# Performance work log

Hardware: AMD Instinct MI355X
Metric: run time of the kernel (lower is better)

The kernel has to match this reference:

```python
import jax, jax.numpy as jnp
import numpy as np
from jax import lax

K_NN = 16      # neighbors used by compute_knn_distance
ANCHOR_K = 64  # config['anchor_k']


def _knn_dist_vec(pts):
    """compute_knn_distance for one object: mean offset vector to K_NN nearest neighbors.
    pts: (N, 3) -> (N, 3)"""
    sq = jnp.sum(pts * pts, axis=-1)                      # (N,)
    d2 = sq[:, None] + sq[None, :] - 2.0 * (pts @ pts.T)  # (N, N) squared dists
    n = pts.shape[0]
    d2 = d2 + jnp.eye(n, dtype=pts.dtype) * 1e10          # exclude self
    _, idx = lax.top_k(-d2, K_NN)                          # (N, K_NN) nearest indices
    neigh = pts[idx]                                       # (N, K_NN, 3)
    return jnp.mean(neigh - pts[:, None, :], axis=1)       # (N, 3)


def _fps(pts, k):
    """Farthest point sampling for one object. pts: (N, 3) -> (k,) int32 indices."""
    d0 = jnp.sum((pts - pts[0]) ** 2, axis=-1)             # dist to seed point 0

    def step(min_d, _):
        idx = jnp.argmax(min_d)
        d = jnp.sum((pts - pts[idx]) ** 2, axis=-1)
        return jnp.minimum(min_d, d), idx

    _, idxs = lax.scan(step, d0, None, length=k - 1)
    return jnp.concatenate([jnp.zeros((1,), dtype=idxs.dtype), idxs])


def setup_inputs() -> dict:
    key = jax.random.key(0)
    k1, k2, k3, k4 = jax.random.split(key, 4)
    B, N_obj, N_v = 4, 8, 2048
    positions = jax.random.normal(k1, (B, N_obj, N_v, 3), dtype=jnp.float32)
    velocities = jax.random.normal(k2, (B, N_obj, N_v, 3), dtype=jnp.float32)
    physics_params = jax.random.uniform(k3, (B, N_obj, 3), dtype=jnp.float32)
    # reference pose at t=0: nearby but distinct so rel_pos is nontrivial
    ref_positions = positions + 0.05 * jax.random.normal(k4, (B, N_obj, N_v, 3), dtype=jnp.float32)
    return {"positions": positions, "velocities": velocities,
            "physics_params": physics_params, "ref_positions": ref_positions}


def reference(positions, velocities, physics_params, ref_positions):
    B, N_obj, N_v, _ = positions.shape
    flat = positions.reshape(B * N_obj, N_v, 3)

    # pairwise KNN distance feature per point
    dist_vec = jax.vmap(_knn_dist_vec)(flat).reshape(B, N_obj, N_v, 3)

    # iterative FPS anchor sampling (vectorized over all B*N_obj objects)
    anchors = jax.vmap(lambda p: _fps(p, ANCHOR_K))(flat).reshape(B, N_obj, ANCHOR_K)

    rel_pos = positions - ref_positions

    # multi-field gather at anchor indices (torch.gather on dim=2)
    gather = lambda f: jnp.take_along_axis(f, anchors[..., None], axis=2)
    anchor_dist = gather(dist_vec)       # (B, N_obj, K, 3)
    anchor_vel = gather(velocities)      # (B, N_obj, K, 3)
    anchor_rel = gather(rel_pos)         # (B, N_obj, K, 3)

    phys = jnp.broadcast_to(physics_params[:, :, None, :], (B, N_obj, ANCHOR_K, 3))
    query = jnp.concatenate([anchor_dist, anchor_vel, anchor_rel, phys], axis=-1)  # (B, N_obj, K, 12)
    return query
```

## Files before the change

### kernel.cpp

```cpp
#include <hip/hip_runtime.h>
#include <stdint.h>

#define NPTS 2048
#define KNN  16
#define AK   64
#define TPB  256
#define FPT  (NPTS / TPB)
#define KPL  (NPTS / 64)

typedef unsigned long long u64;
typedef unsigned int u32;
#define UMAX 0xFFFFFFFFFFFFFFFFull

__device__ __forceinline__ float sq3(float x, float y, float z) {
    return __fadd_rn(__fadd_rn(__fmul_rn(x, x), __fmul_rn(y, y)), __fmul_rn(z, z));
}

template <int CTRL>
__device__ __forceinline__ u64 dpp64(u64 k) {
    const int lo = __builtin_amdgcn_update_dpp((int)(u32)k, (int)(u32)k,
                                               CTRL, 0xF, 0xF, false);
    const int hi = __builtin_amdgcn_update_dpp((int)(u32)(k >> 32),
                                               (int)(u32)(k >> 32),
                                               CTRL, 0xF, 0xF, false);
    return ((u64)(u32)hi << 32) | (u32)lo;
}

__device__ __forceinline__ u64 wave_max64(u64 k) {
    u64 o;
    o = dpp64<0xB1>(k);  if (o > k) k = o;
    o = dpp64<0x4E>(k);  if (o > k) k = o;
    o = dpp64<0x141>(k); if (o > k) k = o;
    o = dpp64<0x140>(k); if (o > k) k = o;
    o = (u64)__shfl_xor((long long)k, 16, 64); if (o > k) k = o;
    o = (u64)__shfl_xor((long long)k, 32, 64); if (o > k) k = o;
    return k;
}

__device__ __forceinline__ u64 wave_min64(u64 k) {
    u64 o;
    o = dpp64<0xB1>(k);  if (o < k) k = o;
    o = dpp64<0x4E>(k);  if (o < k) k = o;
    o = dpp64<0x141>(k); if (o < k) k = o;
    o = dpp64<0x140>(k); if (o < k) k = o;
    o = (u64)__shfl_xor((long long)k, 16, 64); if (o < k) k = o;
    o = (u64)__shfl_xor((long long)k, 32, 64); if (o < k) k = o;
    return k;
}

__global__ __launch_bounds__(TPB) void fps_kernel(const float* __restrict__ pos,
                                                  int* __restrict__ anchors) {
    const int obj = blockIdx.x;
    const int t = threadIdx.x;
    const int wid = t >> 6, lane = t & 63;

    __shared__ float sX[NPTS], sY[NPTS], sZ[NPTS];
    __shared__ u64 skey[8];
    __shared__ float4 scrd[8];

    const float* pts = pos + (size_t)obj * NPTS * 3;
    #pragma unroll
    for (int i = 0; i < FPT; i++) {
        const int j = t + i * TPB;
        sX[j] = pts[j * 3 + 0];
        sY[j] = pts[j * 3 + 1];
        sZ[j] = pts[j * 3 + 2];
    }
    __syncthreads();

    float px[FPT], py[FPT], pz[FPT], mind[FPT];
    u64 key;
    {
        const float ax0 = sX[0], ay0 = sY[0], az0 = sZ[0];
        float bv = -1.0f; u32 bj = 0;
        #pragma unroll
        for (int i = 0; i < FPT; i++) {
            const int j = t + i * TPB;
            px[i] = sX[j]; py[i] = sY[j]; pz[i] = sZ[j];
            const float d2 = sq3(__fsub_rn(px[i], ax0), __fsub_rn(py[i], ay0),
                                 __fsub_rn(pz[i], az0));
            mind[i] = d2;
            if (d2 > bv) { bv = d2; bj = (u32)j; }
        }
        key = ((u64)__float_as_uint(bv) << 32) | (u32)(~bj);
    }
    if (t == 0) anchors[obj * AK + 0] = 0;

    for (int s = 1; s < AK; s++) {
        const u64 wk = wave_max64(key);
        const int side = (s & 1) * 4;
        if (lane == 0) {
            const int widx = (int)(~(u32)wk);
            skey[side + wid] = wk;
            scrd[side + wid] = make_float4(sX[widx], sY[widx], sZ[widx], 0.f);
        }
        __syncthreads();
        u64 ka = skey[side + 0];
        float4 ca = scrd[side + 0];
        { const u64 k1 = skey[side + 1]; const float4 q = scrd[side + 1];
          if (k1 > ka) { ka = k1; ca = q; } }
        { const u64 k2 = skey[side + 2]; const float4 q = scrd[side + 2];
          if (k2 > ka) { ka = k2; ca = q; } }
        { const u64 k3 = skey[side + 3]; const float4 q = scrd[side + 3];
          if (k3 > ka) { ka = k3; ca = q; } }
        if (t == 0) anchors[obj * AK + s] = (int)(~(u32)ka);
        if (s == AK - 1) break;

        float bv = -1.0f; u32 bj = 0;
        #pragma unroll
        for (int i = 0; i < FPT; i++) {
            const float d2 = sq3(__fsub_rn(px[i], ca.x), __fsub_rn(py[i], ca.y),
                                 __fsub_rn(pz[i], ca.z));
            const float nm = fminf(mind[i], d2);
            mind[i] = nm;
            if (nm > bv) { bv = nm; bj = (u32)(t + i * TPB); }
        }
        key = ((u64)__float_as_uint(bv) << 32) | (u32)(~bj);
    }
}

__global__ __launch_bounds__(TPB) void knn_gather_kernel(
    const float* __restrict__ pos, const float* __restrict__ vel,
    const float* __restrict__ phys, const float* __restrict__ refp,
    const int* __restrict__ anchors, float* __restrict__ out) {
    const int t = threadIdx.x;
    const int wid = t >> 6, lane = t & 63;
    const int g = blockIdx.x * 4 + wid;
    const int obj = g >> 6;

    __shared__ float sX[NPTS], sY[NPTS], sZ[NPTS];
    const float* pts = pos + (size_t)obj * NPTS * 3;
    #pragma unroll
    for (int i = 0; i < FPT; i++) {
        const int j = t + i * TPB;
        sX[j] = pts[j * 3 + 0];
        sY[j] = pts[j * 3 + 1];
        sZ[j] = pts[j * 3 + 2];
    }
    const int a = anchors[g];
    __syncthreads();

    const float ax = sX[a], ay = sY[a], az = sZ[a];
    const float sqa = sq3(ax, ay, az);

    u64 k[KPL];
    #pragma unroll
    for (int i = 0; i < KPL; i++) {
        const int j = lane + i * 64;
        const float x = sX[j], y = sY[j], z = sZ[j];
        const float sqj = sq3(x, y, z);
        const float dot = __fadd_rn(
            __fadd_rn(__fmul_rn(ax, x), __fmul_rn(ay, y)), __fmul_rn(az, z));
        const float d2 = __fsub_rn(__fadd_rn(sqa, sqj), __fmul_rn(2.0f, dot));
        u32 bb = __float_as_uint(d2);
        bb ^= (bb & 0x80000000u) ? 0xFFFFFFFFu : 0x80000000u;
        k[i] = (j == a) ? UMAX : (((u64)bb << 32) | (u32)j);
    }

    u64 c0 = UMAX, c1 = UMAX, c2 = UMAX, c3 = UMAX;
    #pragma unroll
    for (int i = 0; i < KPL; i++) c0 = (k[i] < c0) ? k[i] : c0;
    #pragma unroll
    for (int i = 0; i < KPL; i++) {
        const u64 v = (k[i] > c0) ? k[i] : UMAX; c1 = (v < c1) ? v : c1;
    }
    #pragma unroll
    for (int i = 0; i < KPL; i++) {
        const u64 v = (k[i] > c1) ? k[i] : UMAX; c2 = (v < c2) ? v : c2;
    }
    #pragma unroll
    for (int i = 0; i < KPL; i++) {
        const u64 v = (k[i] > c2) ? k[i] : UMAX; c3 = (v < c3) ? v : c3;
    }

    float accx = 0.f, accy = 0.f, accz = 0.f;
    u64 thr = 0;
    for (int r = 0; r < KNN; r++) {
        if (c0 == UMAX) {
            #pragma unroll
            for (int i = 0; i < KPL; i++) {
                const u64 v = (k[i] > thr) ? k[i] : UMAX; c0 = (v < c0) ? v : c0;
            }
            #pragma unroll
            for (int i = 0; i < KPL; i++) {
                const u64 v = (k[i] > c0) ? k[i] : UMAX; c1 = (v < c1) ? v : c1;
            }
            #pragma unroll
            for (int i = 0; i < KPL; i++) {
                const u64 v = (k[i] > c1) ? k[i] : UMAX; c2 = (v < c2) ? v : c2;
            }
            #pragma unroll
            for (int i = 0; i < KPL; i++) {
                const u64 v = (k[i] > c2) ? k[i] : UMAX; c3 = (v < c3) ? v : c3;
            }
        }
        const u64 w = wave_min64(c0);
        const int winj = (int)(u32)w;
        const float wx = sX[winj], wy = sY[winj], wz = sZ[winj];
        accx = __fadd_rn(accx, __fsub_rn(wx, ax));
        accy = __fadd_rn(accy, __fsub_rn(wy, ay));
        accz = __fadd_rn(accz, __fsub_rn(wz, az));
        if (c0 == w) {
            thr = c0; c0 = c1; c1 = c2; c2 = c3; c3 = UMAX;
        }
    }

    if (lane == 0) {
        float* o = out + (size_t)g * 12;
        o[0] = __fmul_rn(accx, 0.0625f);
        o[1] = __fmul_rn(accy, 0.0625f);
        o[2] = __fmul_rn(accz, 0.0625f);
        const size_t base = (size_t)obj * NPTS * 3 + (size_t)a * 3;
        o[3] = vel[base + 0];
        o[4] = vel[base + 1];
        o[5] = vel[base + 2];
        o[6] = __fsub_rn(pos[base + 0], refp[base + 0]);
        o[7] = __fsub_rn(pos[base + 1], refp[base + 1]);
        o[8] = __fsub_rn(pos[base + 2], refp[base + 2]);
        const float* ph = phys + (size_t)obj * 3;
        o[9]  = ph[0];
        o[10] = ph[1];
        o[11] = ph[2];
    }
}

extern "C" void kernel_launch(void* const* d_in, const int* in_sizes, int n_in,
                              void* d_out, int out_size, void* d_ws, size_t ws_size,
                              hipStream_t stream) {
    const float* pos  = (const float*)d_in[0];
    const float* vel  = (const float*)d_in[1];
    const float* phys = (const float*)d_in[2];
    const float* refp = (const float*)d_in[3];
    float* out = (float*)d_out;

    const int n_obj = in_sizes[2] / 3;
    int* anchors = (int*)d_ws;

    fps_kernel<<<n_obj, TPB, 0, stream>>>(pos, anchors);
    knn_gather_kernel<<<n_obj * AK / 4, TPB, 0, stream>>>(pos, vel, phys, refp,
                                                          anchors, out);
}
```

Measured before the change: 109.6 us.

## Carry winner coordinates through DPP reductions, pack float2 math, shrink KNN candidate cache

The FPS kernel no longer stages points in shared memory. It loads each thread's points straight into registers as float2 pairs and carries the winning point's coordinates through the wave max reduction, so the per-step shared-memory coordinate lookup goes away. Wave reductions now use DPP row_bcast with readlane instead of shfl_xor. The KNN kernel computes distances with packed float2 math and keeps two cached candidates per lane instead of four, which cuts the initial selection passes but may trigger more rescans.

```diff
diff --git a/kernel.cpp b/kernel.cpp
--- a/kernel.cpp
+++ b/kernel.cpp
@@ -5,59 +5,157 @@
 #define KNN  16
 #define AK   64
 #define TPB  256
-#define FPT  (NPTS / TPB)
-#define KPL  (NPTS / 64)
+#define FPT  8
+#define FPP  4
+#define KPL  32
+#define KPP  16
 
 typedef unsigned long long u64;
 typedef unsigned int u32;
+typedef __attribute__((ext_vector_type(2))) float v2f;
 #define UMAX 0xFFFFFFFFFFFFFFFFull
 
 __device__ __forceinline__ float sq3(float x, float y, float z) {
     return __fadd_rn(__fadd_rn(__fmul_rn(x, x), __fmul_rn(y, y)), __fmul_rn(z, z));
 }
 
-template <int CTRL>
-__device__ __forceinline__ u64 dpp64(u64 k) {
-    const int lo = __builtin_amdgcn_update_dpp((int)(u32)k, (int)(u32)k,
-                                               CTRL, 0xF, 0xF, false);
-    const int hi = __builtin_amdgcn_update_dpp((int)(u32)(k >> 32),
-                                               (int)(u32)(k >> 32),
-                                               CTRL, 0xF, 0xF, false);
-    return ((u64)(u32)hi << 32) | (u32)lo;
-}
-
-__device__ __forceinline__ u64 wave_max64(u64 k) {
-    u64 o;
-    o = dpp64<0xB1>(k);  if (o > k) k = o;
-    o = dpp64<0x4E>(k);  if (o > k) k = o;
-    o = dpp64<0x141>(k); if (o > k) k = o;
-    o = dpp64<0x140>(k); if (o > k) k = o;
-    o = (u64)__shfl_xor((long long)k, 16, 64); if (o > k) k = o;
-    o = (u64)__shfl_xor((long long)k, 32, 64); if (o > k) k = o;
-    return k;
+template <int CTRL, int RMASK>
+__device__ __forceinline__ u32 dpp32(u32 v) {
+    return (u32)__builtin_amdgcn_update_dpp((int)v, (int)v, CTRL, RMASK, 0xF, false);
+}
+
+template <int CTRL, int RMASK>
+__device__ __forceinline__ void maxstep(u32& lo, u32& hi,
+                                        float& x, float& y, float& z) {
+    const u32 olo = dpp32<CTRL, RMASK>(lo);
+    const u32 ohi = dpp32<CTRL, RMASK>(hi);
+    const u32 ox = dpp32<CTRL, RMASK>(__float_as_uint(x));
+    const u32 oy = dpp32<CTRL, RMASK>(__float_as_uint(y));
+    const u32 oz = dpp32<CTRL, RMASK>(__float_as_uint(z));
+    const u64 a = ((u64)hi << 32) | lo;
+    const u64 b = ((u64)ohi << 32) | olo;
+    if (b > a) {
+        lo = olo; hi = ohi;
+        x = __uint_as_float(ox); y = __uint_as_float(oy); z = __uint_as_float(oz);
+    }
+}
+
+template <int CTRL, int RMASK>
+__device__ __forceinline__ u64 minstep(u64 k) {
+    const u32 olo = dpp32<CTRL, RMASK>((u32)k);
+    const u32 ohi = dpp32<CTRL, RMASK>((u32)(k >> 32));
+    const u64 o = ((u64)ohi << 32) | olo;
+    return (o < k) ? o : k;
 }
 
 __device__ __forceinline__ u64 wave_min64(u64 k) {
-    u64 o;
-    o = dpp64<0xB1>(k);  if (o < k) k = o;
-    o = dpp64<0x4E>(k);  if (o < k) k = o;
-    o = dpp64<0x141>(k); if (o < k) k = o;
-    o = dpp64<0x140>(k); if (o < k) k = o;
-    o = (u64)__shfl_xor((long long)k, 16, 64); if (o < k) k = o;
-    o = (u64)__shfl_xor((long long)k, 32, 64); if (o < k) k = o;
-    return k;
+    k = minstep<0xB1, 0xF>(k);
+    k = minstep<0x4E, 0xF>(k);
+    k = minstep<0x141, 0xF>(k);
+    k = minstep<0x140, 0xF>(k);
+    k = minstep<0x142, 0xA>(k);
+    k = minstep<0x143, 0xC>(k);
+    const u32 lo = (u32)__builtin_amdgcn_readlane((int)(u32)k, 63);
+    const u32 hi = (u32)__builtin_amdgcn_readlane((int)(u32)(k >> 32), 63);
+    return ((u64)hi << 32) | lo;
 }
 
 __global__ __launch_bounds__(TPB) void fps_kernel(const float* __restrict__ pos,
                                                   int* __restrict__ anchors) {
+#pragma clang fp contract(off)
     const int obj = blockIdx.x;
     const int t = threadIdx.x;
     const int wid = t >> 6, lane = t & 63;
-
-    __shared__ float sX[NPTS], sY[NPTS], sZ[NPTS];
+    const float* pts = pos + (size_t)obj * NPTS * 3;
+
     __shared__ u64 skey[8];
     __shared__ float4 scrd[8];
 
+    v2f px[FPP], py[FPP], pz[FPP], mind[FPP];
+    float bv, bx, by, bz;
+    u32 bj;
+    {
+        const float ax0 = pts[0], ay0 = pts[1], az0 = pts[2];
+        bv = -1.0f; bj = 0; bx = by = bz = 0.0f;
+        #pragma unroll
+        for (int i = 0; i < FPP; i++) {
+            const int jA = t + (2 * i) * TPB;
+            const int jB = t + (2 * i + 1) * TPB;
+            v2f X, Y, Z;
+            X.x = pts[jA * 3 + 0]; Y.x = pts[jA * 3 + 1]; Z.x = pts[jA * 3 + 2];
+            X.y = pts[jB * 3 + 0]; Y.y = pts[jB * 3 + 1]; Z.y = pts[jB * 3 + 2];
+            px[i] = X; py[i] = Y; pz[i] = Z;
+            const v2f dx = X - ax0, dy = Y - ay0, dz = Z - az0;
+            const v2f d2 = dx * dx + dy * dy + dz * dz;
+            mind[i] = d2;
+            if (d2.x > bv) { bv = d2.x; bj = (u32)jA; bx = X.x; by = Y.x; bz = Z.x; }
+            if (d2.y > bv) { bv = d2.y; bj = (u32)jB; bx = X.y; by = Y.y; bz = Z.y; }
+        }
+    }
+    if (t == 0) anchors[obj * AK + 0] = 0;
+
+    for (int s = 1; s < AK; s++) {
+        u32 klo = ~bj, khi = __float_as_uint(bv);
+        float wx = bx, wy = by, wz = bz;
+        maxstep<0xB1, 0xF>(klo, khi, wx, wy, wz);
+        maxstep<0x4E, 0xF>(klo, khi, wx, wy, wz);
+        maxstep<0x141, 0xF>(klo, khi, wx, wy, wz);
+        maxstep<0x140, 0xF>(klo, khi, wx, wy, wz);
+        maxstep<0x142, 0xA>(klo, khi, wx, wy, wz);
+        maxstep<0x143, 0xC>(klo, khi, wx, wy, wz);
+        const u32 wlo = (u32)__builtin_amdgcn_readlane((int)klo, 63);
+        const u32 whi = (u32)__builtin_amdgcn_readlane((int)khi, 63);
+        const u32 ux = (u32)__builtin_amdgcn_readlane((int)__float_as_uint(wx), 63);
+        const u32 uy = (u32)__builtin_amdgcn_readlane((int)__float_as_uint(wy), 63);
+        const u32 uz = (u32)__builtin_amdgcn_readlane((int)__float_as_uint(wz), 63);
+
+        const int side = (s & 1) * 4;
+        if (lane == 0) {
+            skey[side + wid] = ((u64)whi << 32) | wlo;
+            scrd[side + wid] = make_float4(__uint_as_float(ux), __uint_as_float(uy),
+                                           __uint_as_float(uz), 0.0f);
+        }
+        __syncthreads();
+
+        u64 ka = skey[side + 0];
+        float4 ca = scrd[side + 0];
+        { const u64 kb = skey[side + 1]; const float4 cb = scrd[side + 1];
+          if (kb > ka) { ka = kb; ca = cb; } }
+        { const u64 kb = skey[side + 2]; const float4 cb = scrd[side + 2];
+          if (kb > ka) { ka = kb; ca = cb; } }
+        { const u64 kb = skey[side + 3]; const float4 cb = scrd[side + 3];
+          if (kb > ka) { ka = kb; ca = cb; } }
+        if (t == 0) anchors[obj * AK + s] = (int)(~(u32)ka);
+        if (s == AK - 1) break;
+
+        bv = -1.0f; bj = 0;
+        #pragma unroll
+        for (int i = 0; i < FPP; i++) {
+            const v2f dx = px[i] - ca.x, dy = py[i] - ca.y, dz = pz[i] - ca.z;
+            const v2f d2 = dx * dx + dy * dy + dz * dz;
+            v2f nm;
+            nm.x = fminf(mind[i].x, d2.x);
+            nm.y = fminf(mind[i].y, d2.y);
+            mind[i] = nm;
+            if (nm.x > bv) { bv = nm.x; bj = (u32)(t + (2 * i) * TPB);
+                             bx = px[i].x; by = py[i].x; bz = pz[i].x; }
+            if (nm.y > bv) { bv = nm.y; bj = (u32)(t + (2 * i + 1) * TPB);
+                             bx = px[i].y; by = py[i].y; bz = pz[i].y; }
+        }
+    }
+}
+
+__global__ __launch_bounds__(TPB) void knn_gather_kernel(
+    const float* __restrict__ pos, const float* __restrict__ vel,
+    const float* __restrict__ phys, const float* __restrict__ refp,
+    const int* __restrict__ anchors, float* __restrict__ out) {
+#pragma clang fp contract(off)
+    const int t = threadIdx.x;
+    const int wid = t >> 6, lane = t & 63;
+    const int g = blockIdx.x * 4 + wid;
+    const int obj = g >> 6;
+
+    __shared__ float sX[NPTS], sY[NPTS], sZ[NPTS];
     const float* pts = pos + (size_t)obj * NPTS * 3;
     #pragma unroll
     for (int i = 0; i < FPT; i++) {
@@ -66,77 +164,6 @@
         sY[j] = pts[j * 3 + 1];
         sZ[j] = pts[j * 3 + 2];
     }
-    __syncthreads();
-
-    float px[FPT], py[FPT], pz[FPT], mind[FPT];
-    u64 key;
-    {
-        const float ax0 = sX[0], ay0 = sY[0], az0 = sZ[0];
-        float bv = -1.0f; u32 bj = 0;
-        #pragma unroll
-        for (int i = 0; i < FPT; i++) {
-            const int j = t + i * TPB;
-            px[i] = sX[j]; py[i] = sY[j]; pz[i] = sZ[j];
-            const float d2 = sq3(__fsub_rn(px[i], ax0), __fsub_rn(py[i], ay0),
-                                 __fsub_rn(pz[i], az0));
-            mind[i] = d2;
-            if (d2 > bv) { bv = d2; bj = (u32)j; }
-        }
-        key = ((u64)__float_as_uint(bv) << 32) | (u32)(~bj);
-    }
-    if (t == 0) anchors[obj * AK + 0] = 0;
-
-    for (int s = 1; s < AK; s++) {
-        const u64 wk = wave_max64(key);
-        const int side = (s & 1) * 4;
-        if (lane == 0) {
-            const int widx = (int)(~(u32)wk);
-            skey[side + wid] = wk;
-            scrd[side + wid] = make_float4(sX[widx], sY[widx], sZ[widx], 0.f);
-        }
-        __syncthreads();
-        u64 ka = skey[side + 0];
-        float4 ca = scrd[side + 0];
-        { const u64 k1 = skey[side + 1]; const float4 q = scrd[side + 1];
-          if (k1 > ka) { ka = k1; ca = q; } }
-        { const u64 k2 = skey[side + 2]; const float4 q = scrd[side + 2];
-          if (k2 > ka) { ka = k2; ca = q; } }
-        { const u64 k3 = skey[side + 3]; const float4 q = scrd[side + 3];
-          if (k3 > ka) { ka = k3; ca = q; } }
-        if (t == 0) anchors[obj * AK + s] = (int)(~(u32)ka);
-        if (s == AK - 1) break;
-
-        float bv = -1.0f; u32 bj = 0;
-        #pragma unroll
-        for (int i = 0; i < FPT; i++) {
-            const float d2 = sq3(__fsub_rn(px[i], ca.x), __fsub_rn(py[i], ca.y),
-                                 __fsub_rn(pz[i], ca.z));
-            const float nm = fminf(mind[i], d2);
-            mind[i] = nm;
-            if (nm > bv) { bv = nm; bj = (u32)(t + i * TPB); }
-        }
-        key = ((u64)__float_as_uint(bv) << 32) | (u32)(~bj);
-    }
-}
-
-__global__ __launch_bounds__(TPB) void knn_gather_kernel(
-    const float* __restrict__ pos, const float* __restrict__ vel,
-    const float* __restrict__ phys, const float* __restrict__ refp,
-    const int* __restrict__ anchors, float* __restrict__ out) {
-    const int t = threadIdx.x;
-    const int wid = t >> 6, lane = t & 63;
-    const int g = blockIdx.x * 4 + wid;
-    const int obj = g >> 6;
-
-    __shared__ float sX[NPTS], sY[NPTS], sZ[NPTS];
-    const float* pts = pos + (size_t)obj * NPTS * 3;
-    #pragma unroll
-    for (int i = 0; i < FPT; i++) {
-        const int j = t + i * TPB;
-        sX[j] = pts[j * 3 + 0];
-        sY[j] = pts[j * 3 + 1];
-        sZ[j] = pts[j * 3 + 2];
-    }
     const int a = anchors[g];
     __syncthreads();
 
@@ -145,32 +172,28 @@
 
     u64 k[KPL];
     #pragma unroll
-    for (int i = 0; i < KPL; i++) {
-        const int j = lane + i * 64;
-        const float x = sX[j], y = sY[j], z = sZ[j];
-        const float sqj = sq3(x, y, z);
-        const float dot = __fadd_rn(
-            __fadd_rn(__fmul_rn(ax, x), __fmul_rn(ay, y)), __fmul_rn(az, z));
-        const float d2 = __fsub_rn(__fadd_rn(sqa, sqj), __fmul_rn(2.0f, dot));
-        u32 bb = __float_as_uint(d2);
-        bb ^= (bb & 0x80000000u) ? 0xFFFFFFFFu : 0x80000000u;
-        k[i] = (j == a) ? UMAX : (((u64)bb << 32) | (u32)j);
-    }
-
-    u64 c0 = UMAX, c1 = UMAX, c2 = UMAX, c3 = UMAX;
+    for (int i = 0; i < KPP; i++) {
+        const int jA = lane + (2 * i) * 64, jB = lane + (2 * i + 1) * 64;
+        v2f X, Y, Z;
+        X.x = sX[jA]; Y.x = sY[jA]; Z.x = sZ[jA];
+        X.y = sX[jB]; Y.y = sY[jB]; Z.y = sZ[jB];
+        const v2f sqj = X * X + Y * Y + Z * Z;
+        const v2f dot = ax * X + ay * Y + az * Z;
+        const v2f d2 = (sqa + sqj) - 2.0f * dot;
+        u32 b0 = __float_as_uint(d2.x);
+        b0 ^= (b0 & 0x80000000u) ? 0xFFFFFFFFu : 0x80000000u;
+        u32 b1 = __float_as_uint(d2.y);
+        b1 ^= (b1 & 0x80000000u) ? 0xFFFFFFFFu : 0x80000000u;
+        k[2 * i]     = (jA == a) ? UMAX : (((u64)b0 << 32) | (u32)jA);
+        k[2 * i + 1] = (jB == a) ? UMAX : (((u64)b1 << 32) | (u32)jB);
+    }
+
+    u64 c0 = UMAX, c1 = UMAX;
     #pragma unroll
     for (int i = 0; i < KPL; i++) c0 = (k[i] < c0) ? k[i] : c0;
     #pragma unroll
     for (int i = 0; i < KPL; i++) {
         const u64 v = (k[i] > c0) ? k[i] : UMAX; c1 = (v < c1) ? v : c1;
-    }
-    #pragma unroll
-    for (int i = 0; i < KPL; i++) {
-        const u64 v = (k[i] > c1) ? k[i] : UMAX; c2 = (v < c2) ? v : c2;
-    }
-    #pragma unroll
-    for (int i = 0; i < KPL; i++) {
-        const u64 v = (k[i] > c2) ? k[i] : UMAX; c3 = (v < c3) ? v : c3;
     }
 
     float accx = 0.f, accy = 0.f, accz = 0.f;
@@ -185,23 +208,14 @@
             for (int i = 0; i < KPL; i++) {
                 const u64 v = (k[i] > c0) ? k[i] : UMAX; c1 = (v < c1) ? v : c1;
             }
-            #pragma unroll
-            for (int i = 0; i < KPL; i++) {
-                const u64 v = (k[i] > c1) ? k[i] : UMAX; c2 = (v < c2) ? v : c2;
-            }
-            #pragma unroll
-            for (int i = 0; i < KPL; i++) {
-                const u64 v = (k[i] > c2) ? k[i] : UMAX; c3 = (v < c3) ? v : c3;
-            }
         }
         const u64 w = wave_min64(c0);
         const int winj = (int)(u32)w;
-        const float wx = sX[winj], wy = sY[winj], wz = sZ[winj];
-        accx = __fadd_rn(accx, __fsub_rn(wx, ax));
-        accy = __fadd_rn(accy, __fsub_rn(wy, ay));
-        accz = __fadd_rn(accz, __fsub_rn(wz, az));
+        accx = __fadd_rn(accx, __fsub_rn(sX[winj], ax));
+        accy = __fadd_rn(accy, __fsub_rn(sY[winj], ay));
+        accz = __fadd_rn(accz, __fsub_rn(sZ[winj], az));
         if (c0 == w) {
-            thr = c0; c0 = c1; c1 = c2; c2 = c3; c3 = UMAX;
+            thr = c0; c0 = c1; c1 = UMAX;
         }
     }
 
```

Measured after the change: 127.0 us. +15.9%, slower.
